# Optimization experiments

Hardware: AMD Instinct MI355X
Metric: run time of the kernel (lower is better)

Reference implementation:

```python
import jax, jax.numpy as jnp
import numpy as np

TAU = 0.1
MASK_VAL = 1e9


def setup_inputs() -> dict:
    key = jax.random.key(0)
    ka, kb = jax.random.split(key)
    B, D = 4096, 512
    return {
        "view_a": jax.random.normal(ka, (B, D), dtype=jnp.float32),
        "view_b": jax.random.normal(kb, (B, D), dtype=jnp.float32),
    }


def _l2norm(x):
    return x / jnp.maximum(jnp.linalg.norm(x, axis=-1, keepdims=True), 1e-12)


def reference(view_a, view_b):
    a = _l2norm(view_a)
    b = _l2norm(view_b)
    B = a.shape[0]
    labels = jnp.arange(B)  # start_i = 0 (single device)
    mask = jnp.eye(B, dtype=a.dtype) * MASK_VAL

    logits_aa = a @ a.T / TAU - mask
    logits_bb = b @ b.T / TAU - mask
    logits_ab = a @ b.T / TAU
    logits_ba = b @ a.T / TAU

    full_a = jnp.concatenate([logits_ab, logits_aa], axis=1)  # [B, 2B]
    full_b = jnp.concatenate([logits_ba, logits_bb], axis=1)

    def ce(logits):
        logp = jax.nn.log_softmax(logits, axis=-1)
        return -jnp.mean(jnp.take_along_axis(logp, labels[:, None], axis=-1))

    loss = (ce(full_a) + ce(full_b)) / 2

    pred = jnp.argmax(full_a, axis=-1)
    acc = 100.0 * jnp.sum(pred == labels) / B
    return loss, acc
```

## Files before the change

### kernel.cpp

```cpp
#include <hip/hip_runtime.h>
#include <stdint.h>


#define BN 4096
#define DK 512
#define NSPLIT 16
#define NEG_BIG -1e30f
#define SCL 0.15625f
#define SCL2 0.225396744f
#define C2 14.4269504f
#define TILE_BYTES (64 * DK)

typedef __attribute__((ext_vector_type(16))) float floatx16;
typedef __attribute__((ext_vector_type(8))) int intx8;

__global__ void __launch_bounds__(256) prep_kernel(
    const float* __restrict__ A, const float* __restrict__ Bv,
    unsigned char* __restrict__ An, unsigned char* __restrict__ Bn,
    float* __restrict__ diag, float* __restrict__ out) {
  if (blockIdx.x == 0 && threadIdx.x < 2) out[threadIdx.x] = 0.0f;
  const int w = threadIdx.x >> 6, lane = threadIdx.x & 63;
  const int row = blockIdx.x * 4 + w;
  const float4* pa4 = (const float4*)(A + (size_t)row * DK);
  const float4* pb4 = (const float4*)(Bv + (size_t)row * DK);
  float4 a0 = pa4[lane * 2], a1 = pa4[lane * 2 + 1];
  float4 b0 = pb4[lane * 2], b1 = pb4[lane * 2 + 1];
  float ssa = a0.x * a0.x + a0.y * a0.y + a0.z * a0.z + a0.w * a0.w +
              a1.x * a1.x + a1.y * a1.y + a1.z * a1.z + a1.w * a1.w;
  float ssb = b0.x * b0.x + b0.y * b0.y + b0.z * b0.z + b0.w * b0.w +
              b1.x * b1.x + b1.y * b1.y + b1.z * b1.z + b1.w * b1.w;
  float sab = a0.x * b0.x + a0.y * b0.y + a0.z * b0.z + a0.w * b0.w +
              a1.x * b1.x + a1.y * b1.y + a1.z * b1.z + a1.w * b1.w;
#pragma unroll
  for (int off = 32; off > 0; off >>= 1) {
    ssa += __shfl_xor(ssa, off);
    ssb += __shfl_xor(ssb, off);
    sab += __shfl_xor(sab, off);
  }
  float na = fmaxf(sqrtf(ssa), 1e-12f);
  float nb = fmaxf(sqrtf(ssb), 1e-12f);
  const float s = 8.0f;
  float sa = s / na, sb = s / nb;
  const int doff = (lane >> 2) * 32 + (lane & 1) * 16 + ((lane >> 1) & 1) * 8;
  {
    int v0 = __builtin_amdgcn_cvt_pk_fp8_f32(a0.x * sa, a0.y * sa, 0, false);
    v0 = __builtin_amdgcn_cvt_pk_fp8_f32(a0.z * sa, a0.w * sa, v0, true);
    int v1 = __builtin_amdgcn_cvt_pk_fp8_f32(a1.x * sa, a1.y * sa, 0, false);
    v1 = __builtin_amdgcn_cvt_pk_fp8_f32(a1.z * sa, a1.w * sa, v1, true);
    int2 pv; pv.x = v0; pv.y = v1;
    *(int2*)(An + (size_t)row * DK + doff) = pv;
  }
  {
    int v0 = __builtin_amdgcn_cvt_pk_fp8_f32(b0.x * sb, b0.y * sb, 0, false);
    v0 = __builtin_amdgcn_cvt_pk_fp8_f32(b0.z * sb, b0.w * sb, v0, true);
    int v1 = __builtin_amdgcn_cvt_pk_fp8_f32(b1.x * sb, b1.y * sb, 0, false);
    v1 = __builtin_amdgcn_cvt_pk_fp8_f32(b1.z * sb, b1.w * sb, v1, true);
    int2 pv; pv.x = v0; pv.y = v1;
    *(int2*)(Bn + (size_t)row * DK + doff) = pv;
  }
  if (lane == 0) diag[row] = (sab / (na * nb)) * 10.0f;
}

__global__ void __launch_bounds__(256, 2) tiles_kernel(
    const unsigned char* __restrict__ An, const unsigned char* __restrict__ Bn,
    float* __restrict__ pSA, float* __restrict__ pMA, float* __restrict__ pSB) {
  __shared__ __align__(16) unsigned char smem[2 * TILE_BYTES];

  const int rb = blockIdx.x;
  const int split = blockIdx.y;
  const int tid = threadIdx.x;
  const int lane = tid & 63, w = tid >> 6;
  const int n5 = lane & 31, h = lane >> 5;
  const int r0 = rb * 128;
  const int myrow = r0 + w * 32 + n5;

  intx8 aw[8];
  auto loadfrags = [&](const unsigned char* base) {
    const unsigned char* p = base + (size_t)myrow * DK + h * 16;
#pragma unroll
    for (int i = 0; i < 8; ++i) {
      int4 c0 = *(const int4*)(p + i * 64);
      int4 c1 = *(const int4*)(p + i * 64 + 32);
      intx8 v = {c0.x, c0.y, c0.z, c0.w, c1.x, c1.y, c1.z, c1.w};
      aw[i] = v;
    }
  };

  float l[16], mx[16];
#pragma unroll
  for (int r = 0; r < 16; ++r) { l[r] = 0.f; mx[r] = NEG_BIG; }

  auto stage = [&](unsigned char* buf, int jt) {
    const unsigned char* csrc = (jt < 64) ? An : Bn;
    const int cb = (jt & 63) * 64;
#pragma unroll
    for (int ii = 0; ii < 8; ++ii) {
      const int cp = w * 8 + ii;
      const int cl = cp * 2 + h;
      const unsigned char* src =
          csrc + (size_t)(cb + cl) * DK + ((n5 ^ (cl & 7)) * 16);
      __builtin_amdgcn_global_load_lds(
          (const __attribute__((address_space(1))) void*)src,
          (__attribute__((address_space(3))) void*)(buf + cp * 1024),
          16, 0, 0);
    }
  };

  stage(smem, split * 8);
  loadfrags(An);
  __syncthreads();

  const int swz = n5 & 7;
  for (int u = 0; u < 16; ++u) {
    const int t = u & 7;
    const int jt = split * 8 + t;
    unsigned char* cur = smem + (u & 1) * TILE_BYTES;
    unsigned char* nxt = smem + ((u + 1) & 1) * TILE_BYTES;
    if (u < 15) stage(nxt, split * 8 + ((t + 1) & 7));

    floatx16 acc[2];
#pragma unroll
    for (int cs = 0; cs < 2; ++cs)
#pragma unroll
      for (int r = 0; r < 16; ++r) acc[cs][r] = 0.f;

    const unsigned char* bbase = cur + (size_t)n5 * DK;
#pragma unroll
    for (int i = 0; i < 8; ++i) {
      const int p1 = ((4 * i + h) ^ swz) * 16;
      const int p2 = ((4 * i + 2 + h) ^ swz) * 16;
#pragma unroll
      for (int cs = 0; cs < 2; ++cs) {
        int4 b0 = *(const int4*)(bbase + cs * 32 * DK + p1);
        int4 b1 = *(const int4*)(bbase + cs * 32 * DK + p2);
        intx8 bw = {b0.x, b0.y, b0.z, b0.w, b1.x, b1.y, b1.z, b1.w};
        acc[cs] = __builtin_amdgcn_mfma_scale_f32_32x32x64_f8f6f4(
            aw[i], bw, acc[cs], 0, 0, 0, 0x7F7F7F7F, 0, 0x7F7F7F7F);
      }
    }

    const bool dtile = (((jt & 63) >> 1) == rb);
    const int colbase = (jt & 63) * 64;
    const bool passA = (u < 8);
#pragma unroll
    for (int r = 0; r < 16; ++r) {
      float v0 = acc[0][r], v1 = acc[1][r];
      if (dtile) {
        const int rowg = r0 + w * 32 + (r & 3) + 8 * (r >> 2) + 4 * h;
        if (rowg == colbase + n5)      v0 = NEG_BIG;
        if (rowg == colbase + 32 + n5) v1 = NEG_BIG;
      }
      if (passA) mx[r] = fmaxf(mx[r], fmaxf(v0, v1));
      l[r] += exp2f(fmaf(v0, SCL2, -C2)) + exp2f(fmaf(v1, SCL2, -C2));
    }

    if (u == 7) {
#pragma unroll
      for (int off = 1; off < 32; off <<= 1)
#pragma unroll
        for (int r = 0; r < 16; ++r) {
          l[r] += __shfl_xor(l[r], off);
          mx[r] = fmaxf(mx[r], __shfl_xor(mx[r], off));
        }
      if (n5 == 0) {
#pragma unroll
        for (int r = 0; r < 16; ++r) {
          const int row = r0 + w * 32 + (r & 3) + 8 * (r >> 2) + 4 * h;
          pSA[split * BN + row] = l[r];
          pMA[split * BN + row] = mx[r] * SCL;
        }
      }
#pragma unroll
      for (int r = 0; r < 16; ++r) l[r] = 0.f;
      loadfrags(Bn);
    }
    __syncthreads();
  }

#pragma unroll
  for (int off = 1; off < 32; off <<= 1)
#pragma unroll
    for (int r = 0; r < 16; ++r) l[r] += __shfl_xor(l[r], off);
  if (n5 == 0) {
#pragma unroll
    for (int r = 0; r < 16; ++r) {
      const int row = r0 + w * 32 + (r & 3) + 8 * (r >> 2) + 4 * h;
      pSB[split * BN + row] = l[r];
    }
  }
}

__global__ void __launch_bounds__(256) finalize_kernel(
    const float* __restrict__ pSA, const float* __restrict__ pMA,
    const float* __restrict__ pSB, const float* __restrict__ diag,
    float* __restrict__ out) {
  const int row = blockIdx.x * 256 + threadIdx.x;
  float SA = 0.f, SB = 0.f, MA = NEG_BIG;
#pragma unroll
  for (int s = 0; s < NSPLIT; ++s) {
    SA += pSA[s * BN + row];
    SB += pSB[s * BN + row];
    MA = fmaxf(MA, pMA[s * BN + row]);
  }
  const float d = diag[row];
  const float eL = exp2f(fmaf(d, 1.44269504f, -C2));
  float lseA = 10.0f + logf(SA + eL);
  float lseB = 10.0f + logf(SB + eL);
  float lossi = (lseA - d) + (lseB - d);
  float corr = (d >= MA) ? 1.f : 0.f;
#pragma unroll
  for (int off = 32; off > 0; off >>= 1) {
    lossi += __shfl_xor(lossi, off);
    corr += __shfl_xor(corr, off);
  }
  __shared__ float sred[2][4];
  if ((threadIdx.x & 63) == 0) {
    int w = threadIdx.x >> 6;
    sred[0][w] = lossi; sred[1][w] = corr;
  }
  __syncthreads();
  if (threadIdx.x == 0) {
    float ls = sred[0][0] + sred[0][1] + sred[0][2] + sred[0][3];
    float cs = sred[1][0] + sred[1][1] + sred[1][2] + sred[1][3];
    atomicAdd(&out[0], ls * (1.0f / 8192.0f));
    atomicAdd(&out[1], cs * (100.0f / 4096.0f));
  }
}

extern "C" void kernel_launch(void* const* d_in, const int* in_sizes, int n_in,
                              void* d_out, int out_size, void* d_ws, size_t ws_size,
                              hipStream_t stream) {
  const float* A = (const float*)d_in[0];
  const float* Bv = (const float*)d_in[1];
  unsigned char* An = (unsigned char*)d_ws;
  unsigned char* Bn = An + (size_t)BN * DK;
  float* diag = (float*)(Bn + (size_t)BN * DK);
  float* pSA = diag + BN;
  float* pMA = pSA + NSPLIT * BN;
  float* pSB = pMA + NSPLIT * BN;
  float* out = (float*)d_out;

  prep_kernel<<<BN / 4, 256, 0, stream>>>(A, Bv, An, Bn, diag, out);
  tiles_kernel<<<dim3(32, 16), 256, 0, stream>>>(An, Bn, pSA, pMA, pSB);
  finalize_kernel<<<BN / 256, 256, 0, stream>>>(pSA, pMA, pSB, diag, out);
}
```

Measured before the change: 124.4 us.

## Process A and B rows together against shared column tiles with 4-stage pipeline

The tiles kernel now keeps both A-row and B-row FP8 fragments in registers. Each 32-column tile staged in LDS feeds two MFMAs, one for the A rows and one for the B rows, instead of running two passes over the same columns. Staging moves to a 4-buffer ring with explicit vmcnt waits and raw barriers in place of a double buffer with __syncthreads, and MFMA priority is raised during compute. The goal is to halve LDS tile loads per MFMA and hide global-to-LDS latency better, at the cost of higher register pressure from holding both fragment sets.

```diff
diff --git a/kernel.cpp b/kernel.cpp
--- a/kernel.cpp
+++ b/kernel.cpp
@@ -5,11 +5,12 @@
 #define BN 4096
 #define DK 512
 #define NSPLIT 16
+#define NT 16
 #define NEG_BIG -1e30f
 #define SCL 0.15625f
 #define SCL2 0.225396744f
 #define C2 14.4269504f
-#define TILE_BYTES (64 * DK)
+#define TILE_BYTES (32 * DK)
 
 typedef __attribute__((ext_vector_type(16))) float floatx16;
 typedef __attribute__((ext_vector_type(8))) int intx8;
@@ -64,7 +65,7 @@
 __global__ void __launch_bounds__(256, 2) tiles_kernel(
     const unsigned char* __restrict__ An, const unsigned char* __restrict__ Bn,
     float* __restrict__ pSA, float* __restrict__ pMA, float* __restrict__ pSB) {
-  __shared__ __align__(16) unsigned char smem[2 * TILE_BYTES];
+  __shared__ __align__(16) unsigned char smem[4 * TILE_BYTES];
 
   const int rb = blockIdx.x;
   const int split = blockIdx.y;
@@ -73,32 +74,39 @@
   const int n5 = lane & 31, h = lane >> 5;
   const int r0 = rb * 128;
   const int myrow = r0 + w * 32 + n5;
-
-  intx8 aw[8];
-  auto loadfrags = [&](const unsigned char* base) {
-    const unsigned char* p = base + (size_t)myrow * DK + h * 16;
+  const int csplit = split & 7;
+  const unsigned char* __restrict__ csrc = (split < 8) ? An : Bn;
+
+  intx8 ar[8], br[8];
+  {
+    const unsigned char* pa = An + (size_t)myrow * DK + h * 16;
+    const unsigned char* pb = Bn + (size_t)myrow * DK + h * 16;
 #pragma unroll
     for (int i = 0; i < 8; ++i) {
-      int4 c0 = *(const int4*)(p + i * 64);
-      int4 c1 = *(const int4*)(p + i * 64 + 32);
-      intx8 v = {c0.x, c0.y, c0.z, c0.w, c1.x, c1.y, c1.z, c1.w};
-      aw[i] = v;
-    }
-  };
-
-  float l[16], mx[16];
-#pragma unroll
-  for (int r = 0; r < 16; ++r) { l[r] = 0.f; mx[r] = NEG_BIG; }
-
-  auto stage = [&](unsigned char* buf, int jt) {
-    const unsigned char* csrc = (jt < 64) ? An : Bn;
-    const int cb = (jt & 63) * 64;
-#pragma unroll
-    for (int ii = 0; ii < 8; ++ii) {
-      const int cp = w * 8 + ii;
+      int4 c0 = *(const int4*)(pa + i * 64);
+      int4 c1 = *(const int4*)(pa + i * 64 + 32);
+      intx8 va = {c0.x, c0.y, c0.z, c0.w, c1.x, c1.y, c1.z, c1.w};
+      ar[i] = va;
+      int4 d0 = *(const int4*)(pb + i * 64);
+      int4 d1 = *(const int4*)(pb + i * 64 + 32);
+      intx8 vb = {d0.x, d0.y, d0.z, d0.w, d1.x, d1.y, d1.z, d1.w};
+      br[i] = vb;
+    }
+  }
+
+  float la[16], lb[16], mx[16];
+#pragma unroll
+  for (int r = 0; r < 16; ++r) { la[r] = 0.f; lb[r] = 0.f; mx[r] = NEG_BIG; }
+
+  auto stage = [&](int bu, int t) {
+    unsigned char* buf = smem + bu * TILE_BYTES;
+    const int cb = csplit * 512 + t * 32;
+#pragma unroll
+    for (int ii = 0; ii < 4; ++ii) {
+      const int cp = w * 4 + ii;
       const int cl = cp * 2 + h;
       const unsigned char* src =
-          csrc + (size_t)(cb + cl) * DK + ((n5 ^ (cl & 7)) * 16);
+          csrc + (size_t)(cb + cl) * DK + ((n5 ^ cl) * 16);
       __builtin_amdgcn_global_load_lds(
           (const __attribute__((address_space(1))) void*)src,
           (__attribute__((address_space(3))) void*)(buf + cp * 1024),
@@ -106,86 +114,72 @@
     }
   };
 
-  stage(smem, split * 8);
-  loadfrags(An);
-  __syncthreads();
-
-  const int swz = n5 & 7;
-  for (int u = 0; u < 16; ++u) {
-    const int t = u & 7;
-    const int jt = split * 8 + t;
-    unsigned char* cur = smem + (u & 1) * TILE_BYTES;
-    unsigned char* nxt = smem + ((u + 1) & 1) * TILE_BYTES;
-    if (u < 15) stage(nxt, split * 8 + ((t + 1) & 7));
-
-    floatx16 acc[2];
-#pragma unroll
-    for (int cs = 0; cs < 2; ++cs)
-#pragma unroll
-      for (int r = 0; r < 16; ++r) acc[cs][r] = 0.f;
-
-    const unsigned char* bbase = cur + (size_t)n5 * DK;
+  stage(0, 0);
+  stage(1, 1);
+  stage(2, 2);
+
+  const unsigned char* bb = smem + (size_t)n5 * DK;
+
+#pragma unroll
+  for (int u = 0; u < NT; ++u) {
+    if (u <= NT - 3)      asm volatile("s_waitcnt vmcnt(8)" ::: "memory");
+    else if (u == NT - 2) asm volatile("s_waitcnt vmcnt(4)" ::: "memory");
+    else                  asm volatile("s_waitcnt vmcnt(0)" ::: "memory");
+    __builtin_amdgcn_s_barrier();
+    __builtin_amdgcn_sched_barrier(0);
+    if (u + 3 < NT) stage((u + 3) & 3, u + 3);
+
+    floatx16 ya, yb;
+#pragma unroll
+    for (int r = 0; r < 16; ++r) { ya[r] = 0.f; yb[r] = 0.f; }
+
+    const unsigned char* bt = bb + (u & 3) * TILE_BYTES;
+    __builtin_amdgcn_s_setprio(1);
 #pragma unroll
     for (int i = 0; i < 8; ++i) {
-      const int p1 = ((4 * i + h) ^ swz) * 16;
-      const int p2 = ((4 * i + 2 + h) ^ swz) * 16;
-#pragma unroll
-      for (int cs = 0; cs < 2; ++cs) {
-        int4 b0 = *(const int4*)(bbase + cs * 32 * DK + p1);
-        int4 b1 = *(const int4*)(bbase + cs * 32 * DK + p2);
-        intx8 bw = {b0.x, b0.y, b0.z, b0.w, b1.x, b1.y, b1.z, b1.w};
-        acc[cs] = __builtin_amdgcn_mfma_scale_f32_32x32x64_f8f6f4(
-            aw[i], bw, acc[cs], 0, 0, 0, 0x7F7F7F7F, 0, 0x7F7F7F7F);
-      }
-    }
-
-    const bool dtile = (((jt & 63) >> 1) == rb);
-    const int colbase = (jt & 63) * 64;
-    const bool passA = (u < 8);
+      const int p1 = ((4 * i + h) ^ n5) * 16;
+      const int p2 = ((4 * i + 2 + h) ^ n5) * 16;
+      int4 c0 = *(const int4*)(bt + p1);
+      int4 c1 = *(const int4*)(bt + p2);
+      intx8 cw = {c0.x, c0.y, c0.z, c0.w, c1.x, c1.y, c1.z, c1.w};
+      ya = __builtin_amdgcn_mfma_scale_f32_32x32x64_f8f6f4(
+          ar[i], cw, ya, 0, 0, 0, 0x7F7F7F7F, 0, 0x7F7F7F7F);
+      yb = __builtin_amdgcn_mfma_scale_f32_32x32x64_f8f6f4(
+          br[i], cw, yb, 0, 0, 0, 0x7F7F7F7F, 0, 0x7F7F7F7F);
+    }
+    __builtin_amdgcn_s_setprio(0);
+
+    const int ct = csplit * 16 + u;
+    const bool dtile = ((ct >> 2) == rb);
+    const int colg = ct * 32 + n5;
 #pragma unroll
     for (int r = 0; r < 16; ++r) {
-      float v0 = acc[0][r], v1 = acc[1][r];
+      float va = ya[r], vb = yb[r];
       if (dtile) {
         const int rowg = r0 + w * 32 + (r & 3) + 8 * (r >> 2) + 4 * h;
-        if (rowg == colbase + n5)      v0 = NEG_BIG;
-        if (rowg == colbase + 32 + n5) v1 = NEG_BIG;
+        if (rowg == colg) { va = NEG_BIG; vb = NEG_BIG; }
       }
-      if (passA) mx[r] = fmaxf(mx[r], fmaxf(v0, v1));
-      l[r] += exp2f(fmaf(v0, SCL2, -C2)) + exp2f(fmaf(v1, SCL2, -C2));
-    }
-
-    if (u == 7) {
-#pragma unroll
-      for (int off = 1; off < 32; off <<= 1)
-#pragma unroll
-        for (int r = 0; r < 16; ++r) {
-          l[r] += __shfl_xor(l[r], off);
-          mx[r] = fmaxf(mx[r], __shfl_xor(mx[r], off));
-        }
-      if (n5 == 0) {
-#pragma unroll
-        for (int r = 0; r < 16; ++r) {
-          const int row = r0 + w * 32 + (r & 3) + 8 * (r >> 2) + 4 * h;
-          pSA[split * BN + row] = l[r];
-          pMA[split * BN + row] = mx[r] * SCL;
-        }
-      }
-#pragma unroll
-      for (int r = 0; r < 16; ++r) l[r] = 0.f;
-      loadfrags(Bn);
-    }
-    __syncthreads();
+      mx[r] = fmaxf(mx[r], va);
+      la[r] += exp2f(fmaf(va, SCL2, -C2));
+      lb[r] += exp2f(fmaf(vb, SCL2, -C2));
+    }
   }
 
 #pragma unroll
   for (int off = 1; off < 32; off <<= 1)
 #pragma unroll
-    for (int r = 0; r < 16; ++r) l[r] += __shfl_xor(l[r], off);
+    for (int r = 0; r < 16; ++r) {
+      la[r] += __shfl_xor(la[r], off);
+      lb[r] += __shfl_xor(lb[r], off);
+      mx[r] = fmaxf(mx[r], __shfl_xor(mx[r], off));
+    }
   if (n5 == 0) {
 #pragma unroll
     for (int r = 0; r < 16; ++r) {
       const int row = r0 + w * 32 + (r & 3) + 8 * (r >> 2) + 4 * h;
-      pSB[split * BN + row] = l[r];
+      pSA[split * BN + row] = la[r];
+      pMA[split * BN + row] = mx[r] * SCL;
+      pSB[split * BN + row] = lb[r];
     }
   }
 }
```

After: 210.3 us. 69.1% more time.

## Fuse finalize into tiles kernel via last-block counter and widen LDS swizzle

Applied to the files above, without the earlier changes.

Removes the separate finalize launch. An atomic counter elects the last finishing tiles block, which reduces the per-split partial sums and writes loss and accuracy directly. The LDS XOR swizzle now spans all 32 16-byte chunks of a row instead of 8, to cut bank conflicts on B-fragment reads. The MFMA section is also wrapped in s_setprio and the outer loop is kept rolled. In exchange, the final reduction runs serially in a single block, and the counter must be reset in the prep kernel on every call.

```diff
diff --git a/kernel.cpp b/kernel.cpp
--- a/kernel.cpp
+++ b/kernel.cpp
@@ -17,8 +17,10 @@
 __global__ void __launch_bounds__(256) prep_kernel(
     const float* __restrict__ A, const float* __restrict__ Bv,
     unsigned char* __restrict__ An, unsigned char* __restrict__ Bn,
-    float* __restrict__ diag, float* __restrict__ out) {
+    float* __restrict__ diag, float* __restrict__ out,
+    unsigned int* __restrict__ cnt) {
   if (blockIdx.x == 0 && threadIdx.x < 2) out[threadIdx.x] = 0.0f;
+  if (blockIdx.x == 0 && threadIdx.x == 2) cnt[0] = 0u;
   const int w = threadIdx.x >> 6, lane = threadIdx.x & 63;
   const int row = blockIdx.x * 4 + w;
   const float4* pa4 = (const float4*)(A + (size_t)row * DK);
@@ -63,8 +65,11 @@
 
 __global__ void __launch_bounds__(256, 2) tiles_kernel(
     const unsigned char* __restrict__ An, const unsigned char* __restrict__ Bn,
-    float* __restrict__ pSA, float* __restrict__ pMA, float* __restrict__ pSB) {
+    float* __restrict__ pSA, float* __restrict__ pMA, float* __restrict__ pSB,
+    const float* __restrict__ diag, float* __restrict__ out,
+    unsigned int* __restrict__ cnt) {
   __shared__ __align__(16) unsigned char smem[2 * TILE_BYTES];
+  __shared__ unsigned int s_last;
 
   const int rb = blockIdx.x;
   const int split = blockIdx.y;
@@ -73,6 +78,8 @@
   const int n5 = lane & 31, h = lane >> 5;
   const int r0 = rb * 128;
   const int myrow = r0 + w * 32 + n5;
+  const int csplit = split & 7;
+  const unsigned char* __restrict__ csrc = (split < 8) ? An : Bn;
 
   intx8 aw[8];
   auto loadfrags = [&](const unsigned char* base) {
@@ -86,19 +93,14 @@
     }
   };
 
-  float l[16], mx[16];
-#pragma unroll
-  for (int r = 0; r < 16; ++r) { l[r] = 0.f; mx[r] = NEG_BIG; }
-
-  auto stage = [&](unsigned char* buf, int jt) {
-    const unsigned char* csrc = (jt < 64) ? An : Bn;
-    const int cb = (jt & 63) * 64;
+  auto stage = [&](unsigned char* buf, int t) {
+    const int cb = csplit * 512 + t * 64;
 #pragma unroll
     for (int ii = 0; ii < 8; ++ii) {
       const int cp = w * 8 + ii;
       const int cl = cp * 2 + h;
       const unsigned char* src =
-          csrc + (size_t)(cb + cl) * DK + ((n5 ^ (cl & 7)) * 16);
+          csrc + (size_t)(cb + cl) * DK + ((n5 ^ (cl & 31)) * 16);
       __builtin_amdgcn_global_load_lds(
           (const __attribute__((address_space(1))) void*)src,
           (__attribute__((address_space(3))) void*)(buf + cp * 1024),
@@ -106,45 +108,51 @@
     }
   };
 
-  stage(smem, split * 8);
+  float l[16], mx[16];
+#pragma unroll
+  for (int r = 0; r < 16; ++r) { l[r] = 0.f; mx[r] = NEG_BIG; }
+
   loadfrags(An);
+  stage(smem, 0);
   __syncthreads();
 
-  const int swz = n5 & 7;
+#pragma unroll 1
   for (int u = 0; u < 16; ++u) {
     const int t = u & 7;
-    const int jt = split * 8 + t;
     unsigned char* cur = smem + (u & 1) * TILE_BYTES;
     unsigned char* nxt = smem + ((u + 1) & 1) * TILE_BYTES;
-    if (u < 15) stage(nxt, split * 8 + ((t + 1) & 7));
-
-    floatx16 acc[2];
-#pragma unroll
-    for (int cs = 0; cs < 2; ++cs)
-#pragma unroll
-      for (int r = 0; r < 16; ++r) acc[cs][r] = 0.f;
+    if (u < 15) stage(nxt, (t + 1) & 7);
+
+    floatx16 acc0, acc1;
+#pragma unroll
+    for (int r = 0; r < 16; ++r) { acc0[r] = 0.f; acc1[r] = 0.f; }
 
     const unsigned char* bbase = cur + (size_t)n5 * DK;
+    __builtin_amdgcn_s_setprio(1);
 #pragma unroll
     for (int i = 0; i < 8; ++i) {
-      const int p1 = ((4 * i + h) ^ swz) * 16;
-      const int p2 = ((4 * i + 2 + h) ^ swz) * 16;
-#pragma unroll
-      for (int cs = 0; cs < 2; ++cs) {
-        int4 b0 = *(const int4*)(bbase + cs * 32 * DK + p1);
-        int4 b1 = *(const int4*)(bbase + cs * 32 * DK + p2);
-        intx8 bw = {b0.x, b0.y, b0.z, b0.w, b1.x, b1.y, b1.z, b1.w};
-        acc[cs] = __builtin_amdgcn_mfma_scale_f32_32x32x64_f8f6f4(
-            aw[i], bw, acc[cs], 0, 0, 0, 0x7F7F7F7F, 0, 0x7F7F7F7F);
-      }
-    }
-
-    const bool dtile = (((jt & 63) >> 1) == rb);
-    const int colbase = (jt & 63) * 64;
+      const int p1 = ((4 * i + h) ^ n5) * 16;
+      const int p2 = ((4 * i + 2 + h) ^ n5) * 16;
+      int4 b0 = *(const int4*)(bbase + p1);
+      int4 b1 = *(const int4*)(bbase + p2);
+      intx8 bw = {b0.x, b0.y, b0.z, b0.w, b1.x, b1.y, b1.z, b1.w};
+      acc0 = __builtin_amdgcn_mfma_scale_f32_32x32x64_f8f6f4(
+          aw[i], bw, acc0, 0, 0, 0, 0x7F7F7F7F, 0, 0x7F7F7F7F);
+      int4 c0 = *(const int4*)(bbase + 32 * DK + p1);
+      int4 c1 = *(const int4*)(bbase + 32 * DK + p2);
+      intx8 cw = {c0.x, c0.y, c0.z, c0.w, c1.x, c1.y, c1.z, c1.w};
+      acc1 = __builtin_amdgcn_mfma_scale_f32_32x32x64_f8f6f4(
+          aw[i], cw, acc1, 0, 0, 0, 0x7F7F7F7F, 0, 0x7F7F7F7F);
+    }
+    __builtin_amdgcn_s_setprio(0);
+
+    const int ct = csplit * 8 + t;
+    const bool dtile = ((ct >> 1) == rb);
+    const int colbase = ct * 64;
     const bool passA = (u < 8);
 #pragma unroll
     for (int r = 0; r < 16; ++r) {
-      float v0 = acc[0][r], v1 = acc[1][r];
+      float v0 = acc0[r], v1 = acc1[r];
       if (dtile) {
         const int rowg = r0 + w * 32 + (r & 3) + 8 * (r >> 2) + 4 * h;
         if (rowg == colbase + n5)      v0 = NEG_BIG;
@@ -188,42 +196,42 @@
       pSB[split * BN + row] = l[r];
     }
   }
-}
-
-__global__ void __launch_bounds__(256) finalize_kernel(
-    const float* __restrict__ pSA, const float* __restrict__ pMA,
-    const float* __restrict__ pSB, const float* __restrict__ diag,
-    float* __restrict__ out) {
-  const int row = blockIdx.x * 256 + threadIdx.x;
-  float SA = 0.f, SB = 0.f, MA = NEG_BIG;
-#pragma unroll
-  for (int s = 0; s < NSPLIT; ++s) {
-    SA += pSA[s * BN + row];
-    SB += pSB[s * BN + row];
-    MA = fmaxf(MA, pMA[s * BN + row]);
-  }
-  const float d = diag[row];
-  const float eL = exp2f(fmaf(d, 1.44269504f, -C2));
-  float lseA = 10.0f + logf(SA + eL);
-  float lseB = 10.0f + logf(SB + eL);
-  float lossi = (lseA - d) + (lseB - d);
-  float corr = (d >= MA) ? 1.f : 0.f;
-#pragma unroll
-  for (int off = 32; off > 0; off >>= 1) {
-    lossi += __shfl_xor(lossi, off);
-    corr += __shfl_xor(corr, off);
-  }
-  __shared__ float sred[2][4];
-  if ((threadIdx.x & 63) == 0) {
-    int w = threadIdx.x >> 6;
-    sred[0][w] = lossi; sred[1][w] = corr;
-  }
+
+  __threadfence();
+  if (tid == 0) s_last = (atomicAdd(cnt, 1u) == (32u * 16u - 1u));
   __syncthreads();
-  if (threadIdx.x == 0) {
-    float ls = sred[0][0] + sred[0][1] + sred[0][2] + sred[0][3];
-    float cs = sred[1][0] + sred[1][1] + sred[1][2] + sred[1][3];
-    atomicAdd(&out[0], ls * (1.0f / 8192.0f));
-    atomicAdd(&out[1], cs * (100.0f / 4096.0f));
+  if (s_last) {
+    __threadfence();
+    float lsum = 0.f, csum = 0.f;
+#pragma unroll 1
+    for (int it = 0; it < 16; ++it) {
+      const int row = it * 256 + tid;
+      float SA = 0.f, SB = 0.f, MA = NEG_BIG;
+#pragma unroll
+      for (int s = 0; s < NSPLIT; ++s) {
+        SA += pSA[s * BN + row];
+        SB += pSB[s * BN + row];
+        MA = fmaxf(MA, pMA[s * BN + row]);
+      }
+      const float d = diag[row];
+      const float eL = exp2f(fmaf(d, 1.44269504f, -C2));
+      lsum += (10.0f + logf(SA + eL) - d) + (10.0f + logf(SB + eL) - d);
+      csum += (d >= MA) ? 1.f : 0.f;
+    }
+#pragma unroll
+    for (int off = 32; off > 0; off >>= 1) {
+      lsum += __shfl_xor(lsum, off);
+      csum += __shfl_xor(csum, off);
+    }
+    float* sm = (float*)smem;
+    if (lane == 0) { sm[w] = lsum; sm[4 + w] = csum; }
+    __syncthreads();
+    if (tid == 0) {
+      const float ls = sm[0] + sm[1] + sm[2] + sm[3];
+      const float cs = sm[4] + sm[5] + sm[6] + sm[7];
+      out[0] = ls * (1.0f / 8192.0f);
+      out[1] = cs * (100.0f / 4096.0f);
+    }
   }
 }
 
@@ -238,9 +246,10 @@
   float* pSA = diag + BN;
   float* pMA = pSA + NSPLIT * BN;
   float* pSB = pMA + NSPLIT * BN;
+  unsigned int* cnt = (unsigned int*)(pSB + NSPLIT * BN);
   float* out = (float*)d_out;
 
-  prep_kernel<<<BN / 4, 256, 0, stream>>>(A, Bv, An, Bn, diag, out);
-  tiles_kernel<<<dim3(32, 16), 256, 0, stream>>>(An, Bn, pSA, pMA, pSB);
-  finalize_kernel<<<BN / 256, 256, 0, stream>>>(pSA, pMA, pSB, diag, out);
+  prep_kernel<<<BN / 4, 256, 0, stream>>>(A, Bv, An, Bn, diag, out, cnt);
+  tiles_kernel<<<dim3(32, 16), 256, 0, stream>>>(An, Bn, pSA, pMA, pSB,
+                                                 diag, out, cnt);
 }
```

Result: slower. 163.9 us (+31.8%).
